# Kernel tuning notes

Measured on AMD Instinct MI355X. Metric: run time of the kernel, lower is better.

The kernel has to match this reference:

```python
import jax, jax.numpy as jnp
import numpy as np

B, SQ, QD = 8, 4096, 1280
SCTX, CD = 93, 2048
HEADS, DIM_HEAD = 20, 64
INNER = HEADS * DIM_HEAD  # 1280


def setup_inputs() -> dict:
    key = jax.random.key(0)
    ks = jax.random.split(key, 10)
    inp = {
        'x': jax.random.normal(ks[0], (B, SQ, QD), dtype=jnp.float32),
        'context': jax.random.normal(ks[1], (B, SCTX, CD), dtype=jnp.float32),
        'scale': jax.random.uniform(ks[2], (), dtype=jnp.float32),
        'num_img_token': 16,
        # learned parameters (PyTorch nn.Linear weight layout: [out, in])
        'Wq': jax.random.normal(ks[3], (INNER, QD), dtype=jnp.float32) * 0.02,
        'Wk': jax.random.normal(ks[4], (INNER, CD), dtype=jnp.float32) * 0.02,
        'Wv': jax.random.normal(ks[5], (INNER, CD), dtype=jnp.float32) * 0.02,
        'Wk_ip': jax.random.normal(ks[6], (INNER, CD), dtype=jnp.float32) * 0.02,
        'Wv_ip': jax.random.normal(ks[7], (INNER, CD), dtype=jnp.float32) * 0.02,
        'Wout': jax.random.normal(ks[8], (QD, INNER), dtype=jnp.float32) * 0.02,
        'b_out': jax.random.normal(ks[9], (QD,), dtype=jnp.float32) * 0.02,
    }
    return inp


def _heads(t):
    # [b, s, inner] -> [b, h, s, d]
    b, s, _ = t.shape
    return t.reshape(b, s, HEADS, DIM_HEAD).transpose(0, 2, 1, 3)


def _attn(q, k, v):
    # q: [b,h,sq,d], k/v: [b,h,skv,d]
    sm_scale = 1.0 / jnp.sqrt(jnp.asarray(DIM_HEAD, q.dtype))
    logits = jnp.einsum('bhqd,bhkd->bhqk', q, k) * sm_scale
    probs = jax.nn.softmax(logits, axis=-1)
    return jnp.einsum('bhqk,bhkd->bhqd', probs, v)


def reference(x, context, scale, num_img_token, Wq, Wk, Wv, Wk_ip, Wv_ip, Wout, b_out):
    eos = context.shape[1] - num_img_token
    txt_ctx = context[:, :eos, :]
    img_ctx = context[:, eos:, :]

    q = _heads(jnp.einsum('bsc,ic->bsi', x, Wq))
    k = _heads(jnp.einsum('bsc,ic->bsi', txt_ctx, Wk))
    v = _heads(jnp.einsum('bsc,ic->bsi', txt_ctx, Wv))
    k_i = _heads(jnp.einsum('bsc,ic->bsi', img_ctx, Wk_ip))
    v_i = _heads(jnp.einsum('bsc,ic->bsi', img_ctx, Wv_ip))

    txt_out = _attn(q, k, v)            # [b,h,sq,d]
    img_out = _attn(q, k_i, v_i)        # [b,h,sq,d]
    out = txt_out + scale * img_out

    out = out.transpose(0, 2, 1, 3).reshape(x.shape[0], x.shape[1], INNER)
    return jnp.einsum('bsi,oi->bso', out, Wout) + b_out
```

## Files before the change

kernel.cpp:

```cpp
#include <hip/hip_runtime.h>
#include <stdint.h>
#include <stddef.h>

typedef __attribute__((ext_vector_type(8))) short bf16x8;
typedef __attribute__((ext_vector_type(4))) short bf16x4;
typedef __attribute__((ext_vector_type(4))) float f32x4;

typedef const __attribute__((address_space(1))) uint32_t gas_u32;
typedef __attribute__((address_space(3))) uint32_t las_u32;

__device__ __forceinline__ short f2bf(float f) {
  union { float f; uint32_t u; } c; c.f = f;
  uint32_t u = c.u;
  u += 0x7fffu + ((u >> 16) & 1u);
  return (short)(u >> 16);
}

__global__ void k_cvt(const float* __restrict__ src, short* __restrict__ dst, int n) {
  int i = (blockIdx.x * 256 + threadIdx.x) * 4;
  if (i + 4 <= n) {
    float4 v = *(const float4*)(src + i);
    bf16x4 o = { f2bf(v.x), f2bf(v.y), f2bf(v.z), f2bf(v.w) };
    *(bf16x4*)(dst + i) = o;
  } else {
    for (; i < n; ++i) dst[i] = f2bf(src[i]);
  }
}

__global__ void k_cvt_ctx(const float* __restrict__ ctx, short* __restrict__ dst,
                          int rpb, int row0) {
  long total = 8L * rpb * 2048;
  long i = ((long)blockIdx.x * 256 + threadIdx.x) * 4;
  if (i >= total) return;
  int c = (int)(i & 2047);
  long rs = i >> 11;
  int b = (int)(rs / rpb);
  int s = (int)(rs - (long)b * rpb);
  const float* sp = ctx + ((long)(b * 93 + row0 + s) * 2048 + c);
  float4 v = *(const float4*)sp;
  bf16x4 o = { f2bf(v.x), f2bf(v.y), f2bf(v.z), f2bf(v.w) };
  *(bf16x4*)(dst + i) = o;
}

struct GFrag { bf16x8 a[4]; bf16x8 b[4]; };

__device__ __forceinline__ void g_ld(GFrag& f, const short* as, const short* bs,
                                     int wm, int wn, int r16, int swz) {
#pragma unroll
  for (int i = 0; i < 4; ++i)
    f.a[i] = *(const bf16x8*)(as + (wm + i * 16 + r16) * 32 + swz);
#pragma unroll
  for (int j = 0; j < 4; ++j)
    f.b[j] = *(const bf16x8*)(bs + (wn + j * 16 + r16) * 32 + swz);
}

__device__ __forceinline__ void g_mm(const GFrag& f, f32x4 acc[4][4]) {
#pragma unroll
  for (int i = 0; i < 4; ++i)
#pragma unroll
    for (int j = 0; j < 4; ++j)
      acc[i][j] = __builtin_amdgcn_mfma_f32_16x16x32_bf16(f.a[i], f.b[j], acc[i][j], 0, 0, 0);
}

__device__ __forceinline__ void g_stage(short* asd, short* bsd,
                                        const short* ga0, const short* ga1,
                                        const short* gb0, const short* gb1,
                                        int k0, int p0, int p1) {
  __builtin_amdgcn_global_load_lds((gas_u32*)(ga0 + k0), (las_u32*)(asd + p0 * 8), 16, 0, 0);
  __builtin_amdgcn_global_load_lds((gas_u32*)(ga1 + k0), (las_u32*)(asd + p1 * 8), 16, 0, 0);
  __builtin_amdgcn_global_load_lds((gas_u32*)(gb0 + k0), (las_u32*)(bsd + p0 * 8), 16, 0, 0);
  __builtin_amdgcn_global_load_lds((gas_u32*)(gb1 + k0), (las_u32*)(bsd + p1 * 8), 16, 0, 0);
}

template <int MODE>
__global__ __launch_bounds__(256)
void k_gemm(const short* __restrict__ A, const short* __restrict__ Bm,
            void* __restrict__ out, const float* __restrict__ bias,
            int Mreal, int N, int K, int SPB) {
  __shared__ __align__(16) short As[2][128 * 32];
  __shared__ __align__(16) short Bs[2][128 * 32];
  const int t = threadIdx.x;
  const int lane = t & 63, wave = t >> 6;
  const int wm = (wave >> 1) * 64, wn = (wave & 1) * 64;

  const int nwg = gridDim.x * gridDim.y;
  const int lin = blockIdx.y * gridDim.x + blockIdx.x;
  const int qq = nwg >> 3, r8 = nwg & 7;
  const int xcd = lin & 7, idx = lin >> 3;
  const int wg = (xcd < r8 ? xcd * (qq + 1) : r8 * (qq + 1) + (xcd - r8) * qq) + idx;
  const int bx = wg % gridDim.x, by = wg / gridDim.x;
  const int m0 = by * 128, n0 = bx * 128;
  const int q4 = lane >> 4, r16 = lane & 15;

  f32x4 zero = {0.f, 0.f, 0.f, 0.f};
  f32x4 acc[4][4];
#pragma unroll
  for (int i = 0; i < 4; ++i)
#pragma unroll
    for (int j = 0; j < 4; ++j) acc[i][j] = zero;

  const int p0 = t, p1 = t + 256;
  const int ar0 = p0 >> 2, ac0 = (((p0 & 3) ^ ((ar0 >> 1) & 3))) * 8;
  const int ar1 = p1 >> 2, ac1 = (((p1 & 3) ^ ((ar1 >> 1) & 3))) * 8;
  int gm0 = m0 + ar0; if (gm0 >= Mreal) gm0 = Mreal - 1;
  int gm1 = m0 + ar1; if (gm1 >= Mreal) gm1 = Mreal - 1;
  const short* ga0 = A + (size_t)gm0 * K + ac0;
  const short* ga1 = A + (size_t)gm1 * K + ac1;
  const short* gb0 = Bm + (size_t)(n0 + ar0) * K + ac0;
  const short* gb1 = Bm + (size_t)(n0 + ar1) * K + ac1;

  const int swz = (q4 ^ ((r16 >> 1) & 3)) * 8;

  g_stage(&As[0][0], &Bs[0][0], ga0, ga1, gb0, gb1, 0, p0, p1);
  __syncthreads();

  GFrag f;
  for (int k0 = 32; k0 < K - 32; k0 += 64) {
    g_ld(f, &As[0][0], &Bs[0][0], wm, wn, r16, swz);
    g_stage(&As[1][0], &Bs[1][0], ga0, ga1, gb0, gb1, k0, p0, p1);
    g_mm(f, acc);
    __syncthreads();

    g_ld(f, &As[1][0], &Bs[1][0], wm, wn, r16, swz);
    g_stage(&As[0][0], &Bs[0][0], ga0, ga1, gb0, gb1, k0 + 32, p0, p1);
    g_mm(f, acc);
    __syncthreads();
  }
  g_ld(f, &As[0][0], &Bs[0][0], wm, wn, r16, swz);
  g_stage(&As[1][0], &Bs[1][0], ga0, ga1, gb0, gb1, K - 32, p0, p1);
  g_mm(f, acc);
  __syncthreads();
  g_ld(f, &As[1][0], &Bs[1][0], wm, wn, r16, swz);
  g_mm(f, acc);

  if (MODE == 0) {
    short* O = (short*)out;
#pragma unroll
    for (int i = 0; i < 4; ++i) {
#pragma unroll
      for (int rr = 0; rr < 4; ++rr) {
        int m = m0 + wm + i * 16 + q4 * 4 + rr;
        if (m < Mreal) {
          int bb, ss;
          if (SPB == 4096) { bb = m >> 12; ss = m & 4095; }
          else             { bb = m / SPB; ss = m - bb * SPB; }
#pragma unroll
          for (int j = 0; j < 4; ++j) {
            int n = n0 + wn + j * 16 + r16;
            int h = n >> 6, d = n & 63;
            int grp = (h >= 20) ? 1 : 0;
            int hl = h - grp * 20;
            O[(((size_t)(grp * 160 + bb * 20 + hl)) * SPB + ss) * 64 + d] = f2bf(acc[i][j][rr]);
          }
        }
      }
    }
  } else {
    float* O = (float*)out;
#pragma unroll
    for (int i = 0; i < 4; ++i) {
#pragma unroll
      for (int rr = 0; rr < 4; ++rr) {
        int m = m0 + wm + i * 16 + q4 * 4 + rr;
        if (m < Mreal) {
#pragma unroll
          for (int j = 0; j < 4; ++j) {
            int n = n0 + wn + j * 16 + r16;
            O[(size_t)m * N + n] = acc[i][j][rr] + bias[n];
          }
        }
      }
    }
  }
}

__global__ __launch_bounds__(256)
void k_attn(const short* __restrict__ qb, const short* __restrict__ kb,
            const short* __restrict__ vb, const short* __restrict__ kib,
            const short* __restrict__ vib, const float* __restrict__ scale_p,
            short* __restrict__ out) {
  constexpr int KS = 72;
  constexpr int PS = 104;
  __shared__ __align__(16) short Ks[96 * KS];
  __shared__ __align__(16) short Vt[64 * PS];
  __shared__ __align__(16) short Pp[4][16 * PS];
  const int t = threadIdx.x, lane = t & 63, wave = t >> 6;
  const int q4 = lane >> 4, r16 = lane & 15;
  const int b = blockIdx.z, h = blockIdx.y, qt = blockIdx.x;
  const int bh = b * 20 + h;
  const short* kt = kb + (size_t)bh * 77 * 64;
  const short* vt = vb + (size_t)bh * 77 * 64;
  const short* ki = kib + (size_t)bh * 16 * 64;
  const short* vi = vib + (size_t)bh * 16 * 64;

  for (int c = t; c < 96 * 8; c += 256) {
    int row = c >> 3, o = (c & 7) * 8;
    uint4 val = {0u, 0u, 0u, 0u};
    if (row < 77)       val = *(const uint4*)(kt + row * 64 + o);
    else if (row >= 80) val = *(const uint4*)(ki + (row - 80) * 64 + o);
    *(uint4*)(Ks + row * KS + o) = val;
  }
  for (int i = t; i < 96 * 64; i += 256) {
    int key = i >> 6, d = i & 63;
    short v = 0;
    if (key < 77)       v = vt[key * 64 + d];
    else if (key >= 80) v = vi[(key - 80) * 64 + d];
    Vt[d * PS + key] = v;
  }
  __syncthreads();

  const int s0 = qt * 64 + wave * 16;
  const short* qp = qb + ((size_t)bh * 4096 + s0) * 64;
  bf16x8 qf[2];
#pragma unroll
  for (int kc = 0; kc < 2; ++kc)
    qf[kc] = *(const bf16x8*)(qp + r16 * 64 + kc * 32 + q4 * 8);

  f32x4 zero = {0.f, 0.f, 0.f, 0.f};
  f32x4 lg[6];
#pragma unroll
  for (int nt = 0; nt < 6; ++nt) {
    lg[nt] = zero;
#pragma unroll
    for (int kc = 0; kc < 2; ++kc) {
      bf16x8 kf = *(const bf16x8*)(Ks + (nt * 16 + r16) * KS + kc * 32 + q4 * 8);
      lg[nt] = __builtin_amdgcn_mfma_f32_16x16x32_bf16(qf[kc], kf, lg[nt], 0, 0, 0);
    }
  }

  const float sm = 0.125f;
  const float scl = scale_p[0];
#pragma unroll
  for (int nt = 0; nt < 6; ++nt)
#pragma unroll
    for (int rr = 0; rr < 4; ++rr) lg[nt][rr] *= sm;
  if (r16 >= 13) {
#pragma unroll
    for (int rr = 0; rr < 4; ++rr) lg[4][rr] = -1e30f;
  }

#pragma unroll
  for (int rr = 0; rr < 4; ++rr) {
    float mx = -1e30f;
#pragma unroll
    for (int nt = 0; nt < 5; ++nt) mx = fmaxf(mx, lg[nt][rr]);
#pragma unroll
    for (int o = 1; o < 16; o <<= 1) mx = fmaxf(mx, __shfl_xor(mx, o, 64));
    float s = 0.f;
#pragma unroll
    for (int nt = 0; nt < 5; ++nt) {
      float p = __expf(lg[nt][rr] - mx);
      lg[nt][rr] = p; s += p;
    }
#pragma unroll
    for (int o = 1; o < 16; o <<= 1) s += __shfl_xor(s, o, 64);
    float inv = 1.f / s;
#pragma unroll
    for (int nt = 0; nt < 5; ++nt) lg[nt][rr] *= inv;

    float mi = lg[5][rr];
#pragma unroll
    for (int o = 1; o < 16; o <<= 1) mi = fmaxf(mi, __shfl_xor(mi, o, 64));
    float pi = __expf(lg[5][rr] - mi);
    float si = pi;
#pragma unroll
    for (int o = 1; o < 16; o <<= 1) si += __shfl_xor(si, o, 64);
    lg[5][rr] = pi * (scl / si);
  }

  short* pw = &Pp[wave][0];
#pragma unroll
  for (int nt = 0; nt < 6; ++nt)
#pragma unroll
    for (int rr = 0; rr < 4; ++rr)
      pw[(q4 * 4 + rr) * PS + nt * 16 + r16] = f2bf(lg[nt][rr]);

  f32x4 oc[4];
#pragma unroll
  for (int dt = 0; dt < 4; ++dt) {
    oc[dt] = zero;
#pragma unroll
    for (int kc = 0; kc < 3; ++kc) {
      bf16x8 pf = *(const bf16x8*)(pw + r16 * PS + kc * 32 + q4 * 8);
      bf16x8 vf = *(const bf16x8*)(Vt + (dt * 16 + r16) * PS + kc * 32 + q4 * 8);
      oc[dt] = __builtin_amdgcn_mfma_f32_16x16x32_bf16(pf, vf, oc[dt], 0, 0, 0);
    }
  }

#pragma unroll
  for (int dt = 0; dt < 4; ++dt)
#pragma unroll
    for (int rr = 0; rr < 4; ++rr) {
      int m = s0 + q4 * 4 + rr;
      int d = dt * 16 + r16;
      out[((size_t)b * 4096 + m) * 1280 + h * 64 + d] = f2bf(oc[dt][rr]);
    }
}

extern "C" void kernel_launch(void* const* d_in, const int* in_sizes, int n_in,
                              void* d_out, int out_size, void* d_ws, size_t ws_size,
                              hipStream_t stream) {
  const float* x    = (const float*)d_in[0];
  const float* ctx  = (const float*)d_in[1];
  const float* scal = (const float*)d_in[2];
  const float* Wq   = (const float*)d_in[4];
  const float* Wk   = (const float*)d_in[5];
  const float* Wv   = (const float*)d_in[6];
  const float* Wkip = (const float*)d_in[7];
  const float* Wvip = (const float*)d_in[8];
  const float* Wout = (const float*)d_in[9];
  const float* bout = (const float*)d_in[10];
  float* out = (float*)d_out;

  char* ws = (char*)d_ws;
  size_t off = 0;
  auto alloc = [&](size_t elems) -> short* {
    short* p = (short*)(ws + off);
    off += (elems * 2 + 255) & ~(size_t)255;
    return p;
  };
  short* xb    = alloc(32768UL * 1280);
  short* txtb  = alloc(616UL * 2048);
  short* imgb  = alloc(128UL * 2048);
  short* Wqb   = alloc(1280UL * 1280);
  short* Wkvb  = alloc(2UL * 1280 * 2048);
  short* Wkvip = alloc(2UL * 1280 * 2048);
  short* Woutb = alloc(1280UL * 1280);
  short* qb    = alloc(32768UL * 1280);
  short* kb    = alloc(2UL * 160 * 77 * 64);
  short* kib   = alloc(2UL * 160 * 16 * 64);
  short* vb    = kb  + 160UL * 77 * 64;
  short* vib   = kib + 160UL * 16 * 64;
  short* attnb = xb;

  auto cvt = [&](const float* s, short* d, long n) {
    int blocks = (int)((n / 4 + 255) / 256);
    k_cvt<<<blocks, 256, 0, stream>>>(s, d, (int)n);
  };
  cvt(x, xb, 32768L * 1280);
  cvt(Wq, Wqb, 1280L * 1280);
  cvt(Wk,   Wkvb,                 1280L * 2048);
  cvt(Wv,   Wkvb + 1280L * 2048,  1280L * 2048);
  cvt(Wkip, Wkvip,                1280L * 2048);
  cvt(Wvip, Wkvip + 1280L * 2048, 1280L * 2048);
  cvt(Wout, Woutb, 1280L * 1280);
  {
    long n1 = 8L * 77 * 2048;
    k_cvt_ctx<<<(int)((n1 / 4 + 255) / 256), 256, 0, stream>>>(ctx, txtb, 77, 0);
    long n2 = 8L * 16 * 2048;
    k_cvt_ctx<<<(int)((n2 / 4 + 255) / 256), 256, 0, stream>>>(ctx, imgb, 16, 77);
  }

  { dim3 g(10, 256); k_gemm<0><<<g, 256, 0, stream>>>(xb, Wqb, qb, nullptr, 32768, 1280, 1280, 4096); }
  { dim3 g(20, 5);
    k_gemm<0><<<g, 256, 0, stream>>>(txtb, Wkvb, kb, nullptr, 616, 2560, 2048, 77); }
  { dim3 g(20, 1);
    k_gemm<0><<<g, 256, 0, stream>>>(imgb, Wkvip, kib, nullptr, 128, 2560, 2048, 16); }
  { dim3 g(64, 20, 8);
    k_attn<<<g, 256, 0, stream>>>(qb, kb, vb, kib, vib, scal, attnb); }
  { dim3 g(10, 256);
    k_gemm<1><<<g, 256, 0, stream>>>(attnb, Woutb, out, bout, 32768, 1280, 1280, 1); }
}
```

Baseline: 823.1 us.

## Use 256x256-tile 512-thread GEMM with XCD-aware block remap for Q and output projections

Adds a new GEMM kernel with 256x256 output tiles, 8 waves per block, double-buffered LDS filled by direct global-to-LDS loads, and an interleaved barrier/setprio schedule that overlaps prefetch with MFMA. Block indices are remapped so neighbouring tiles land on the same XCD for better L2 reuse. The large Q projection and output projection switch to this kernel, aiming for higher arithmetic intensity and fewer global loads per FLOP. In exchange it uses 128KB of LDS per block, which limits occupancy and makes the 2-blocks-per-CU launch bound hard to meet, and it needs more registers for the larger accumulator.

```diff
diff --git a/kernel.cpp b/kernel.cpp
--- a/kernel.cpp
+++ b/kernel.cpp
@@ -168,6 +168,139 @@
             int n = n0 + wn + j * 16 + r16;
             O[(size_t)m * N + n] = acc[i][j][rr] + bias[n];
           }
+        }
+      }
+    }
+  }
+}
+
+template <int MODE>
+__global__ __launch_bounds__(512, 2)
+void k_gemm256(const short* __restrict__ A, const short* __restrict__ Bm,
+               void* __restrict__ out, const float* __restrict__ bias,
+               int M, int N, int K, int SPB) {
+  __shared__ __align__(16) short As[2][256 * 64];
+  __shared__ __align__(16) short Bs[2][256 * 64];
+  const int t = threadIdx.x;
+  const int lane = t & 63;
+  const int wave = t >> 6;
+  const int q4 = lane >> 4, r16 = lane & 15;
+  const int wm = (wave >> 2) * 128;
+  const int wn = (wave & 3) * 64;
+
+  const int nwg = gridDim.x * gridDim.y;
+  const int lin = blockIdx.y * gridDim.x + blockIdx.x;
+  const int cpx = nwg >> 3;
+  const int wg = (lin & 7) * cpx + (lin >> 3);
+  const int bx = wg % gridDim.x, by = wg / gridDim.x;
+  const int m0 = by * 256, n0 = bx * 256;
+
+  const int srow = t >> 3;
+  const int csrc = (t & 7) ^ (srow & 7);
+  const short* gA = A + (size_t)(m0 + srow) * K + csrc * 8;
+  const short* gB = Bm + (size_t)(n0 + srow) * K + csrc * 8;
+  const size_t rstep = (size_t)64 * K;
+
+  const int swz0 = ((q4) ^ (r16 & 7)) * 8;
+  const int swz1 = ((4 + q4) ^ (r16 & 7)) * 8;
+
+  f32x4 zero = {0.f, 0.f, 0.f, 0.f};
+  f32x4 acc[8][4];
+#pragma unroll
+  for (int i = 0; i < 8; ++i)
+#pragma unroll
+    for (int j = 0; j < 4; ++j) acc[i][j] = zero;
+
+  auto stageA = [&](short* buf, int k0) {
+    __builtin_amdgcn_global_load_lds((gas_u32*)(gA + k0),             (las_u32*)(buf + (t          ) * 8), 16, 0, 0);
+    __builtin_amdgcn_global_load_lds((gas_u32*)(gA + rstep + k0),     (las_u32*)(buf + (t +  512   ) * 8), 16, 0, 0);
+    __builtin_amdgcn_global_load_lds((gas_u32*)(gA + 2 * rstep + k0), (las_u32*)(buf + (t + 1024   ) * 8), 16, 0, 0);
+    __builtin_amdgcn_global_load_lds((gas_u32*)(gA + 3 * rstep + k0), (las_u32*)(buf + (t + 1536   ) * 8), 16, 0, 0);
+  };
+  auto stageB = [&](short* buf, int k0) {
+    __builtin_amdgcn_global_load_lds((gas_u32*)(gB + k0),             (las_u32*)(buf + (t          ) * 8), 16, 0, 0);
+    __builtin_amdgcn_global_load_lds((gas_u32*)(gB + rstep + k0),     (las_u32*)(buf + (t +  512   ) * 8), 16, 0, 0);
+    __builtin_amdgcn_global_load_lds((gas_u32*)(gB + 2 * rstep + k0), (las_u32*)(buf + (t + 1024   ) * 8), 16, 0, 0);
+    __builtin_amdgcn_global_load_lds((gas_u32*)(gB + 3 * rstep + k0), (las_u32*)(buf + (t + 1536   ) * 8), 16, 0, 0);
+  };
+
+  auto tile = [&](const short* ca, const short* cb, bool pf, int k0n,
+                  short* na, short* nb) {
+    bf16x8 bfr[4][2];
+#pragma unroll
+    for (int q = 0; q < 4; ++q) {
+      if (q == 0) {
+#pragma unroll
+        for (int j = 0; j < 4; ++j) {
+          bfr[j][0] = *(const bf16x8*)(cb + (wn + j * 16 + r16) * 64 + swz0);
+          bfr[j][1] = *(const bf16x8*)(cb + (wn + j * 16 + r16) * 64 + swz1);
+        }
+        if (pf) stageA(na, k0n);
+      }
+      if (q == 1 && pf) stageB(nb, k0n);
+      bf16x8 a0k0 = *(const bf16x8*)(ca + (wm + (2 * q    ) * 16 + r16) * 64 + swz0);
+      bf16x8 a0k1 = *(const bf16x8*)(ca + (wm + (2 * q    ) * 16 + r16) * 64 + swz1);
+      bf16x8 a1k0 = *(const bf16x8*)(ca + (wm + (2 * q + 1) * 16 + r16) * 64 + swz0);
+      bf16x8 a1k1 = *(const bf16x8*)(ca + (wm + (2 * q + 1) * 16 + r16) * 64 + swz1);
+      __builtin_amdgcn_s_barrier();
+      __builtin_amdgcn_s_setprio(1);
+#pragma unroll
+      for (int j = 0; j < 4; ++j) {
+        acc[2 * q][j]     = __builtin_amdgcn_mfma_f32_16x16x32_bf16(a0k0, bfr[j][0], acc[2 * q][j], 0, 0, 0);
+        acc[2 * q][j]     = __builtin_amdgcn_mfma_f32_16x16x32_bf16(a0k1, bfr[j][1], acc[2 * q][j], 0, 0, 0);
+        acc[2 * q + 1][j] = __builtin_amdgcn_mfma_f32_16x16x32_bf16(a1k0, bfr[j][0], acc[2 * q + 1][j], 0, 0, 0);
+        acc[2 * q + 1][j] = __builtin_amdgcn_mfma_f32_16x16x32_bf16(a1k1, bfr[j][1], acc[2 * q + 1][j], 0, 0, 0);
+      }
+      __builtin_amdgcn_s_setprio(0);
+      if (q < 3) __builtin_amdgcn_s_barrier();
+    }
+  };
+
+  stageA(&As[0][0], 0);
+  stageB(&Bs[0][0], 0);
+  __syncthreads();
+
+  const int NT = K >> 6;
+  for (int kt = 0; kt < NT; kt += 2) {
+    const int k1 = (kt + 1) << 6;
+    tile(&As[0][0], &Bs[0][0], k1 < K, k1, &As[1][0], &Bs[1][0]);
+    __syncthreads();
+    const int k2 = (kt + 2) << 6;
+    tile(&As[1][0], &Bs[1][0], k2 < K, k2, &As[0][0], &Bs[0][0]);
+    __syncthreads();
+  }
+
+  if (MODE == 0) {
+    short* O = (short*)out;
+#pragma unroll
+    for (int i = 0; i < 8; ++i) {
+#pragma unroll
+      for (int rr = 0; rr < 4; ++rr) {
+        int m = m0 + wm + i * 16 + q4 * 4 + rr;
+        int bb, ss;
+        if (SPB == 4096) { bb = m >> 12; ss = m & 4095; }
+        else             { bb = m / SPB; ss = m - bb * SPB; }
+#pragma unroll
+        for (int j = 0; j < 4; ++j) {
+          int n = n0 + wn + j * 16 + r16;
+          int h = n >> 6, d = n & 63;
+          int grp = (h >= 20) ? 1 : 0;
+          int hl = h - grp * 20;
+          O[(((size_t)(grp * 160 + bb * 20 + hl)) * SPB + ss) * 64 + d] = f2bf(acc[i][j][rr]);
+        }
+      }
+    }
+  } else {
+    float* O = (float*)out;
+#pragma unroll
+    for (int i = 0; i < 8; ++i) {
+#pragma unroll
+      for (int rr = 0; rr < 4; ++rr) {
+        int m = m0 + wm + i * 16 + q4 * 4 + rr;
+#pragma unroll
+        for (int j = 0; j < 4; ++j) {
+          int n = n0 + wn + j * 16 + r16;
+          O[(size_t)m * N + n] = acc[i][j][rr] + bias[n];
         }
       }
     }
@@ -351,13 +484,13 @@
     k_cvt_ctx<<<(int)((n2 / 4 + 255) / 256), 256, 0, stream>>>(ctx, imgb, 16, 77);
   }
 
-  { dim3 g(10, 256); k_gemm<0><<<g, 256, 0, stream>>>(xb, Wqb, qb, nullptr, 32768, 1280, 1280, 4096); }
+  { dim3 g(5, 128); k_gemm256<0><<<g, 512, 0, stream>>>(xb, Wqb, qb, nullptr, 32768, 1280, 1280, 4096); }
   { dim3 g(20, 5);
     k_gemm<0><<<g, 256, 0, stream>>>(txtb, Wkvb, kb, nullptr, 616, 2560, 2048, 77); }
   { dim3 g(20, 1);
     k_gemm<0><<<g, 256, 0, stream>>>(imgb, Wkvip, kib, nullptr, 128, 2560, 2048, 16); }
   { dim3 g(64, 20, 8);
     k_attn<<<g, 256, 0, stream>>>(qb, kb, vb, kib, vib, scal, attnb); }
-  { dim3 g(10, 256);
-    k_gemm<1><<<g, 256, 0, stream>>>(attnb, Woutb, out, bout, 32768, 1280, 1280, 1); }
-}
+  { dim3 g(5, 128);
+    k_gemm256<1><<<g, 512, 0, stream>>>(attnb, Woutb, out, bout, 32768, 1280, 1280, 1); }
+}
```

Result: faster. 784.1 us (-4.7%).
